# Kernel tuning notes

Hardware: AMD Instinct MI355X
Metric: run time of the kernel (lower is better)

## Reference

```python
import jax, jax.numpy as jnp
import numpy as np
import math

EMB = 1024
H = 8          # num_heads
HD = EMB // H // 2  # head_dim = 64
LAMBDA_INIT = 0.8
B, N = 2, 2048


def setup_inputs() -> dict:
    key = jax.random.key(0)
    ks = jax.random.split(key, 16)
    s = 1.0 / math.sqrt(EMB)
    d = {
        'q': jax.random.normal(ks[0], (B, N, EMB), jnp.float32),
        'k': jax.random.normal(ks[1], (B, N, EMB), jnp.float32),
        'v': jax.random.normal(ks[2], (B, N, EMB), jnp.float32),
        'Wq': jax.random.uniform(ks[3], (EMB, EMB), jnp.float32, -s, s),
        'bq': jax.random.uniform(ks[4], (EMB,), jnp.float32, -s, s),
        'Wk': jax.random.uniform(ks[5], (EMB, EMB), jnp.float32, -s, s),
        'bk': jax.random.uniform(ks[6], (EMB,), jnp.float32, -s, s),
        'Wv': jax.random.uniform(ks[7], (EMB, EMB), jnp.float32, -s, s),
        'bv': jax.random.uniform(ks[8], (EMB,), jnp.float32, -s, s),
        'Wo': jax.random.uniform(ks[9], (EMB, EMB), jnp.float32, -s, s),
        'bo': jax.random.uniform(ks[10], (EMB,), jnp.float32, -s, s),
        'lambda_q1': 0.1 * jax.random.normal(ks[11], (HD,), jnp.float32),
        'lambda_k1': 0.1 * jax.random.normal(ks[12], (HD,), jnp.float32),
        'lambda_q2': 0.1 * jax.random.normal(ks[13], (HD,), jnp.float32),
        'lambda_k2': 0.1 * jax.random.normal(ks[14], (HD,), jnp.float32),
    }
    return d


def reference(q, k, v, Wq, bq, Wk, bk, Wv, bv, Wo, bo,
              lambda_q1, lambda_k1, lambda_q2, lambda_k2):
    b, n, _ = q.shape
    # projections (torch Linear: x @ W.T + b)
    qp = q @ Wq.T + bq            # [b, n, EMB]
    kp = k @ Wk.T + bk
    vp = v @ Wv.T + bv
    # split into 2*H sub-heads of width HD for q/k; H heads of width 2*HD for v
    qh = qp.reshape(b, n, 2 * H, HD).transpose(0, 2, 1, 3)   # [b, 2H, n, HD]
    kh = kp.reshape(b, n, 2 * H, HD).transpose(0, 2, 1, 3)   # [b, 2H, n, HD]
    vh = vp.reshape(b, n, H, 2 * HD).transpose(0, 2, 1, 3)   # [b, H, n, 2HD]
    scale = 1.0 / math.sqrt(HD)
    attn = jnp.einsum('bhqd,bhkd->bhqk', qh, kh) * scale      # [b, 2H, n, n]
    attn = jax.nn.softmax(attn, axis=-1)
    lam1 = jnp.exp(jnp.sum(lambda_q1 * lambda_k1))
    lam2 = jnp.exp(jnp.sum(lambda_q2 * lambda_k2))
    lam = lam1 - lam2 + LAMBDA_INIT
    attn = attn.reshape(b, H, 2, n, n)
    diff = attn[:, :, 0] - lam * attn[:, :, 1]                # [b, H, n, n]
    out = jnp.einsum('bhqk,bhkd->bhqd', diff, vh)             # [b, H, n, 2HD]
    out = out.transpose(0, 2, 1, 3).reshape(b, n, H * 2 * HD)
    return out @ Wo.T + bo
```

## Files before the change

kernel.cpp:

```cpp
#include <hip/hip_runtime.h>
#include <stdint.h>


typedef __attribute__((ext_vector_type(8))) __bf16 bf16x8;
typedef __attribute__((ext_vector_type(4))) __bf16 bf16x4;
typedef __attribute__((ext_vector_type(4))) float f32x4;
typedef __attribute__((ext_vector_type(8))) unsigned short u16x8;
typedef __attribute__((ext_vector_type(4))) unsigned short u16x4;
typedef unsigned short u16;
typedef unsigned int u32;

#define EMB 1024
#define NSEQ 2048
#define NBATCH 2
#define NHEAD 8
#define MROWS (NBATCH*NSEQ)
#define QSCALE 0.18033688011112042f

__device__ __forceinline__ u16x4 pk4(float a, float b, float c, float d){
  bf16x4 h; h[0]=(__bf16)a; h[1]=(__bf16)b; h[2]=(__bf16)c; h[3]=(__bf16)d;
  return __builtin_bit_cast(u16x4, h);
}
__device__ __forceinline__ u16 bf1(float f){
  __bf16 h = (__bf16)f; return __builtin_bit_cast(unsigned short, h);
}

__device__ __forceinline__ bf16x8 ld8(const u16* p){
  return __builtin_bit_cast(bf16x8, *(const u16x8*)p);
}

__device__ __forceinline__ void glds16(const u16* g, u16* l){
  __builtin_amdgcn_global_load_lds(
      (const __attribute__((address_space(1))) u32*)g,
      (__attribute__((address_space(3))) u32*)l, 16, 0, 0);
}

__global__ void cvt_k(const float* __restrict__ q, const float* __restrict__ k,
                      const float* __restrict__ v, const float* __restrict__ Wq,
                      const float* __restrict__ Wk, const float* __restrict__ Wv,
                      const float* __restrict__ Wo,
                      u16* qb, u16* kb, u16* vb, u16* Wqb, u16* Wkb, u16* Wvb, u16* Wob)
{
  const int NQ4 = (NBATCH*NSEQ*EMB)/4;
  const int NW4 = (EMB*EMB)/4;
  const int total = 3*NQ4 + 4*NW4;
  for (int i = blockIdx.x*blockDim.x + threadIdx.x; i < total; i += gridDim.x*blockDim.x){
    const float* src; u16* dst; int off;
    if (i < 3*NQ4){
      int t = i / NQ4; off = i - t*NQ4;
      src = t==0 ? q : (t==1 ? k : v);
      dst = t==0 ? qb : (t==1 ? kb : vb);
    } else {
      int j = i - 3*NQ4;
      int t = j / NW4; off = j - t*NW4;
      src = t==0 ? Wq : (t==1 ? Wk : (t==2 ? Wv : Wo));
      dst = t==0 ? Wqb : (t==1 ? Wkb : (t==2 ? Wvb : Wob));
    }
    f32x4 f = *((const f32x4*)src + off);
    *((u16x4*)dst + off) = pk4(f[0], f[1], f[2], f[3]);
  }
}

__global__ void lambda_k(const float* __restrict__ lq1, const float* __restrict__ lk1,
                         const float* __restrict__ lq2, const float* __restrict__ lk2,
                         float* lam)
{
  int l = threadIdx.x;
  float p1 = lq1[l]*lk1[l];
  float p2 = lq2[l]*lk2[l];
  #pragma unroll
  for (int m=1; m<64; m<<=1){ p1 += __shfl_xor(p1, m, 64); p2 += __shfl_xor(p2, m, 64); }
  if (l==0) lam[0] = __expf(p1) - __expf(p2) + 0.8f;
}

__device__ __forceinline__ void gemm_core(
    const u16* __restrict__ A, const u16* __restrict__ W, const float* __restrict__ bias,
    u16* __restrict__ Ybf, u16* __restrict__ Yvt, float* __restrict__ Yf, int mode,
    float oscale, u16* As, u16* Bs)
{
  const int tid = threadIdx.x, w = tid >> 6, l = tid & 63;
  const int l15 = l & 15, lg = l >> 4;
  const int m0 = blockIdx.y * 128, n0 = blockIdx.x * 128;
  const int wr = w >> 1, wc = w & 1;
  const int srow = w*16 + (l >> 2);
  const int skel = (l & 3) * 8;

  f32x4 acc[4][4] = {};

  for (int kt = 0; kt < EMB/32; ++kt){
    const int kb = kt*32 + skel;
    glds16(A + (size_t)(m0 + srow)*EMB + kb,      As + w*512);
    glds16(A + (size_t)(m0 + 64 + srow)*EMB + kb, As + 2048 + w*512);
    glds16(W + (size_t)(n0 + srow)*EMB + kb,      Bs + w*512);
    glds16(W + (size_t)(n0 + 64 + srow)*EMB + kb, Bs + 2048 + w*512);
    __syncthreads();

    bf16x8 af[4], bfr[4];
    #pragma unroll
    for (int mi=0; mi<4; ++mi) af[mi]  = ld8(As + (wr*64 + mi*16 + l15)*32 + lg*8);
    #pragma unroll
    for (int ni=0; ni<4; ++ni) bfr[ni] = ld8(Bs + (wc*64 + ni*16 + l15)*32 + lg*8);
    #pragma unroll
    for (int mi=0; mi<4; ++mi)
      #pragma unroll
      for (int ni=0; ni<4; ++ni)
        acc[mi][ni] = __builtin_amdgcn_mfma_f32_16x16x32_bf16(af[mi], bfr[ni], acc[mi][ni], 0,0,0);
    __syncthreads();
  }

  #pragma unroll
  for (int mi=0; mi<4; ++mi){
    const int mr = m0 + wr*64 + mi*16 + lg*4;
    #pragma unroll
    for (int ni=0; ni<4; ++ni){
      const int nc = n0 + wc*64 + ni*16 + l15;
      const float bvs = bias[nc]*oscale;
      if (mode == 0){
        #pragma unroll
        for (int i=0;i<4;++i) Ybf[(size_t)(mr+i)*EMB + nc] = bf1(fmaf(acc[mi][ni][i], oscale, bvs));
      } else if (mode == 1){
        const int h = nc >> 7, vd = nc & 127, bb = mr >> 11, t = mr & 2047;
        u16x4 pkv = pk4(acc[mi][ni][0]+bvs, acc[mi][ni][1]+bvs,
                        acc[mi][ni][2]+bvs, acc[mi][ni][3]+bvs);
        *(u16x4*)(Yvt + ((size_t)((bb*NHEAD + h)*128 + vd))*NSEQ + t) = pkv;
      } else {
        #pragma unroll
        for (int i=0;i<4;++i) Yf[(size_t)(mr+i)*EMB + nc] = acc[mi][ni][i] + bvs;
      }
    }
  }
}

__global__ __launch_bounds__(256) void gemm_qkv(
    const u16* qb, const u16* kb, const u16* vb,
    const u16* Wqb, const u16* Wkb, const u16* Wvb,
    const float* bq, const float* bk, const float* bv,
    u16* Qp, u16* Kp, u16* Vt)
{
  __shared__ __align__(16) u16 As[4096], Bs[4096];
  const int z = blockIdx.z;
  const u16* A = z==0 ? qb : (z==1 ? kb : vb);
  const u16* W = z==0 ? Wqb : (z==1 ? Wkb : Wvb);
  const float* bias = z==0 ? bq : (z==1 ? bk : bv);
  if (z == 0)      gemm_core(A, W, bias, Qp, nullptr, nullptr, 0, QSCALE, As, Bs);
  else if (z == 1) gemm_core(A, W, bias, Kp, nullptr, nullptr, 0, 1.0f, As, Bs);
  else             gemm_core(A, W, bias, nullptr, Vt, nullptr, 1, 1.0f, As, Bs);
}

__global__ __launch_bounds__(256) void gemm_out_k(
    const u16* Xc, const u16* Wob, const float* bo, float* out)
{
  __shared__ __align__(16) u16 As[4096], Bs[4096];
  gemm_core(Xc, Wob, bo, nullptr, nullptr, out, 2, 1.0f, As, Bs);
}

__global__ __launch_bounds__(512, 4) void attn_k(
    const u16* __restrict__ Qp, const u16* __restrict__ Kp,
    const u16* __restrict__ Vt, const float* __restrict__ lamp,
    u16* __restrict__ Xc)
{
  __shared__ __align__(16) u16 shm[40960];
  u16* ldsK = shm;
  u16* ldsV = shm + 16384;
  u16* ldsP = shm + 32768;

  const int tid = threadIdx.x, w = tid >> 6, l = tid & 63;
  const int l15 = l & 15, lg = l >> 4;
  const int g = w >> 2, qg = w & 3;
  int bid = blockIdx.x;
  bid = (bid & 7)*64 + (bid >> 3);
  const int qt = bid & 31, bh = bid >> 5;
  const int b = bh >> 3, h = bh & 7;
  const int q0 = qt*64 + qg*16;

  const u16* Kg = Kp + ((size_t)b*NSEQ)*EMB + h*128;
  const u16* Vg = Vt + ((size_t)((b*NHEAD + h)*128))*NSEQ;

  const u16* qbase = Qp + (size_t)(b*NSEQ + q0 + l15)*EMB + 2*h*64;
  bf16x8 qa[2][2];
  #pragma unroll
  for (int s2=0; s2<2; ++s2)
    #pragma unroll
    for (int ks=0; ks<2; ++ks)
      qa[s2][ks] = ld8(qbase + s2*64 + ks*32 + lg*8);

  f32x4 acc[2][8] = {};
  float m_run[2] = {-1e30f, -1e30f}, l_run[2] = {0.f, 0.f};

  u16* Pw = ldsP + w*1024;
  const int sigP = (l15 >> 1) & 3;

  const int kr = l >> 4, kc = l & 15;
  const int vr = l >> 3, vh = (l >> 2) & 1, vs = l & 3;

  auto STAGE = [&](int cur, int t){
    const u16* kg = Kg + ((size_t)t*32)*EMB;
    u16* kd = ldsK + (g*2 + cur)*4096;
    #pragma unroll
    for (int j=0;j<2;++j){
      int row = qg*8 + j*4 + kr;
      glds16(kg + (size_t)row*EMB + ((kc ^ (row&7))*8), kd + (qg*8 + j*4)*128);
    }
    const u16* vg = Vg + t*32;
    u16* vd2 = ldsV + (g*2 + cur)*4096;
    #pragma unroll
    for (int j=0;j<2;++j){
      int row = qg*16 + j*8 + vr;
      glds16(vg + (size_t)(2*row + vh)*NSEQ + ((vs ^ (row&3))*8), vd2 + (qg*16 + j*8)*64);
    }
  };

  STAGE(0, g);
  __syncthreads();
  int cur = 0;

  for (int i = 0; i < 32; ++i){
    const int t = 2*i + g;
    if (i+1 < 32) STAGE(cur^1, t+2);

    const u16* Kb = ldsK + (g*2 + cur)*4096;
    const u16* Vb = ldsV + (g*2 + cur)*4096;

    #pragma unroll
    for (int s2=0; s2<2; ++s2){
      f32x4 st[2] = {};
      __builtin_amdgcn_s_setprio(1);
      #pragma unroll
      for (int nt=0; nt<2; ++nt)
        #pragma unroll
        for (int ks=0; ks<2; ++ks){
          bf16x8 kf = ld8(Kb + (nt*16 + l15)*128 + (((s2*8 + ks*4 + lg) ^ (l15&7))*8));
          st[nt] = __builtin_amdgcn_mfma_f32_16x16x32_bf16(kf, qa[s2][ks], st[nt], 0,0,0);
        }
      __builtin_amdgcn_s_setprio(0);

      float tm = fmaxf(fmaxf(st[0][0], st[0][1]), fmaxf(st[0][2], st[0][3]));
      tm = fmaxf(tm, fmaxf(fmaxf(st[1][0], st[1][1]), fmaxf(st[1][2], st[1][3])));
      tm = fmaxf(tm, __shfl_xor(tm, 16, 64));
      tm = fmaxf(tm, __shfl_xor(tm, 32, 64));
      if (!__all(tm <= m_run[s2] + 11.5f)){
        float mn = fmaxf(m_run[s2], tm);
        float al = exp2f(m_run[s2] - mn);
        m_run[s2] = mn;
        l_run[s2] *= al;
        #pragma unroll
        for (int vt=0; vt<8; ++vt){
          acc[s2][vt][0]*=al; acc[s2][vt][1]*=al; acc[s2][vt][2]*=al; acc[s2][vt][3]*=al;
        }
      }
      float ssum = 0.f;
      #pragma unroll
      for (int nt=0; nt<2; ++nt)
        #pragma unroll
        for (int ii=0; ii<4; ++ii){
          float pv = exp2f(st[nt][ii] - m_run[s2]);
          st[nt][ii] = pv; ssum += pv;
        }
      ssum += __shfl_xor(ssum, 16, 64);
      ssum += __shfl_xor(ssum, 32, 64);
      l_run[s2] += ssum;

      #pragma unroll
      for (int nt=0; nt<2; ++nt){
        u16x4 pkv = pk4(st[nt][0], st[nt][1], st[nt][2], st[nt][3]);
        *(u16x4*)(Pw + s2*512 + l15*32 + (((2*nt + (lg>>1)) ^ sigP)*8) + (lg&1)*4) = pkv;
      }
    }

    bf16x8 pa0 = ld8(Pw +       l15*32 + ((lg ^ sigP)*8));
    bf16x8 pa1 = ld8(Pw + 512 + l15*32 + ((lg ^ sigP)*8));

    __builtin_amdgcn_s_setprio(1);
    #pragma unroll
    for (int vt=0; vt<8; ++vt){
      int r = vt*8 + (l15 >> 1);
      bf16x8 vf = ld8(Vb + r*64 + (l15&1)*32 + ((lg ^ (r&3))*8));
      acc[0][vt] = __builtin_amdgcn_mfma_f32_16x16x32_bf16(vf, pa0, acc[0][vt], 0,0,0);
      acc[1][vt] = __builtin_amdgcn_mfma_f32_16x16x32_bf16(vf, pa1, acc[1][vt], 0,0,0);
    }
    __builtin_amdgcn_s_setprio(0);

    __syncthreads();
    cur ^= 1;
  }

  float* pool = (float*)shm;
  float* ml   = pool + 16896;

  if (g == 1){
    #pragma unroll
    for (int s2=0; s2<2; ++s2){
      #pragma unroll
      for (int vt=0; vt<8; ++vt)
        *(f32x4*)(pool + (size_t)(((qg*2+s2)*16 + l15))*132 + vt*16 + lg*4) = acc[s2][vt];
      if (lg == 0){
        ml[(((qg*2+s2)*16 + l15))*2 + 0] = m_run[s2];
        ml[(((qg*2+s2)*16 + l15))*2 + 1] = l_run[s2];
      }
    }
  }
  __syncthreads();
  if (g == 0){
    const float lam = lamp[0];
    float sc0[2], sc1[2];
    #pragma unroll
    for (int s2=0; s2<2; ++s2){
      float m1 = ml[(((qg*2+s2)*16 + l15))*2 + 0];
      float l1 = ml[(((qg*2+s2)*16 + l15))*2 + 1];
      float M  = fmaxf(m_run[s2], m1);
      float a0 = exp2f(m_run[s2] - M), a1 = exp2f(m1 - M);
      float L  = l_run[s2]*a0 + l1*a1;
      float f  = (s2 == 0) ? 1.f : lam;
      sc0[s2] = f*a0/L; sc1[s2] = f*a1/L;
    }
    #pragma unroll
    for (int vt=0; vt<8; ++vt){
      f32x4 c0 = *(f32x4*)(pool + (size_t)((qg*2+0)*16 + l15)*132 + vt*16 + lg*4);
      f32x4 c1 = *(f32x4*)(pool + (size_t)((qg*2+1)*16 + l15)*132 + vt*16 + lg*4);
      u16x4 o = pk4(
        acc[0][vt][0]*sc0[0] + c0[0]*sc1[0] - acc[1][vt][0]*sc0[1] - c1[0]*sc1[1],
        acc[0][vt][1]*sc0[0] + c0[1]*sc1[0] - acc[1][vt][1]*sc0[1] - c1[1]*sc1[1],
        acc[0][vt][2]*sc0[0] + c0[2]*sc1[0] - acc[1][vt][2]*sc0[1] - c1[2]*sc1[1],
        acc[0][vt][3]*sc0[0] + c0[3]*sc1[0] - acc[1][vt][3]*sc0[1] - c1[3]*sc1[1]);
      *(u16x4*)(Xc + (size_t)(b*NSEQ + q0 + l15)*EMB + h*128 + vt*16 + lg*4) = o;
    }
  }
}

extern "C" void kernel_launch(void* const* d_in, const int* in_sizes, int n_in,
                              void* d_out, int out_size, void* d_ws, size_t ws_size,
                              hipStream_t stream)
{
  const float* q   = (const float*)d_in[0];
  const float* k   = (const float*)d_in[1];
  const float* v   = (const float*)d_in[2];
  const float* Wq  = (const float*)d_in[3];
  const float* bq  = (const float*)d_in[4];
  const float* Wk  = (const float*)d_in[5];
  const float* bk  = (const float*)d_in[6];
  const float* Wv  = (const float*)d_in[7];
  const float* bv  = (const float*)d_in[8];
  const float* Wo  = (const float*)d_in[9];
  const float* bo  = (const float*)d_in[10];
  const float* lq1 = (const float*)d_in[11];
  const float* lk1 = (const float*)d_in[12];
  const float* lq2 = (const float*)d_in[13];
  const float* lk2 = (const float*)d_in[14];

  const size_t NQ = (size_t)MROWS*EMB;
  const size_t NW = (size_t)EMB*EMB;
  u16* qb  = (u16*)d_ws;
  u16* kb  = qb + NQ;
  u16* vb  = kb + NQ;
  u16* Wqb = vb + NQ;
  u16* Wkb = Wqb + NW;
  u16* Wvb = Wkb + NW;
  u16* Wob = Wvb + NW;
  u16* Qp  = Wob + NW;
  u16* Kp  = Qp + NQ;
  u16* Vt  = Kp + NQ;
  u16* Xc  = Vt + NQ;
  float* lam = (float*)(Xc + NQ);

  cvt_k<<<2048, 256, 0, stream>>>(q, k, v, Wq, Wk, Wv, Wo,
                                  qb, kb, vb, Wqb, Wkb, Wvb, Wob);
  lambda_k<<<1, 64, 0, stream>>>(lq1, lk1, lq2, lk2, lam);
  gemm_qkv<<<dim3(EMB/128, MROWS/128, 3), 256, 0, stream>>>(
      qb, kb, vb, Wqb, Wkb, Wvb, bq, bk, bv, Qp, Kp, Vt);
  attn_k<<<dim3(NBATCH*NHEAD*(NSEQ/64)), 512, 0, stream>>>(Qp, Kp, Vt, lam, Xc);
  gemm_out_k<<<dim3(EMB/128, MROWS/128), 256, 0, stream>>>(Xc, Wob, bo, (float*)d_out);
}
```

Measured before the change: 172.7 us.

## Switch attention kernel to 32x32x16 MFMA with register-resident P via permlane swap

Rewrites the attention inner loop to use 32x32x16 bf16 MFMA tiles, with each wave owning one sub-head (s) and 32 query rows instead of both sub-heads over 16 rows. The softmax probabilities are converted with v_cvt_pk_bf16_f32 and rearranged across lanes with v_permlane32_swap, so the P tile stays in registers and the LDS round trip for P is gone. K/V staging swizzles change to match, LDS grows to 66.5 KB, and the epilogue gains extra passes through LDS and extra barriers to combine the two sub-heads with lambda. The larger LDS footprint and higher register use from 4x16 accumulators may reduce occupancy under the (512,4) launch bound.

```diff
diff --git a/kernel.cpp b/kernel.cpp
--- a/kernel.cpp
+++ b/kernel.cpp
@@ -5,8 +5,10 @@
 typedef __attribute__((ext_vector_type(8))) __bf16 bf16x8;
 typedef __attribute__((ext_vector_type(4))) __bf16 bf16x4;
 typedef __attribute__((ext_vector_type(4))) float f32x4;
+typedef __attribute__((ext_vector_type(16))) float f32x16;
 typedef __attribute__((ext_vector_type(8))) unsigned short u16x8;
 typedef __attribute__((ext_vector_type(4))) unsigned short u16x4;
+typedef __attribute__((ext_vector_type(4))) unsigned int u32x4;
 typedef unsigned short u16;
 typedef unsigned int u32;
 
@@ -23,6 +25,9 @@
 }
 __device__ __forceinline__ u16 bf1(float f){
   __bf16 h = (__bf16)f; return __builtin_bit_cast(unsigned short, h);
+}
+__device__ __forceinline__ u32 cvtpk(float lo, float hi){
+  u32 r; asm("v_cvt_pk_bf16_f32 %0, %1, %2" : "=v"(r) : "v"(lo), "v"(hi)); return r;
 }
 
 __device__ __forceinline__ bf16x8 ld8(const u16* p){
@@ -159,54 +164,47 @@
     const u16* __restrict__ Vt, const float* __restrict__ lamp,
     u16* __restrict__ Xc)
 {
-  __shared__ __align__(16) u16 shm[40960];
-  u16* ldsK = shm;
-  u16* ldsV = shm + 16384;
-  u16* ldsP = shm + 32768;
+  __shared__ __align__(16) char shm[66560];
+  u16* ldsK = (u16*)shm;
+  u16* ldsV = (u16*)(shm + 32768);
 
   const int tid = threadIdx.x, w = tid >> 6, l = tid & 63;
-  const int l15 = l & 15, lg = l >> 4;
-  const int g = w >> 2, qg = w & 3;
+  const int l31 = l & 31, hl = l >> 5;
+  const int qg = w & 1, s = (w >> 1) & 1, g = w >> 2;
+  const int wg = w & 3;
   int bid = blockIdx.x;
   bid = (bid & 7)*64 + (bid >> 3);
   const int qt = bid & 31, bh = bid >> 5;
   const int b = bh >> 3, h = bh & 7;
-  const int q0 = qt*64 + qg*16;
+  const int q0 = qt*64 + qg*32;
 
   const u16* Kg = Kp + ((size_t)b*NSEQ)*EMB + h*128;
   const u16* Vg = Vt + ((size_t)((b*NHEAD + h)*128))*NSEQ;
 
-  const u16* qbase = Qp + (size_t)(b*NSEQ + q0 + l15)*EMB + 2*h*64;
-  bf16x8 qa[2][2];
+  {
+  }
+  const u16* qbase = Qp + (size_t)(b*NSEQ + q0 + l31)*EMB + (2*h + s)*64;
+  bf16x8 qa[4];
   #pragma unroll
-  for (int s2=0; s2<2; ++s2)
-    #pragma unroll
-    for (int ks=0; ks<2; ++ks)
-      qa[s2][ks] = ld8(qbase + s2*64 + ks*32 + lg*8);
-
-  f32x4 acc[2][8] = {};
-  float m_run[2] = {-1e30f, -1e30f}, l_run[2] = {0.f, 0.f};
-
-  u16* Pw = ldsP + w*1024;
-  const int sigP = (l15 >> 1) & 3;
-
-  const int kr = l >> 4, kc = l & 15;
-  const int vr = l >> 3, vh = (l >> 2) & 1, vs = l & 3;
+  for (int ks=0; ks<4; ++ks) qa[ks] = ld8(qbase + ks*16 + hl*8);
+
+  f32x16 acc[4] = {};
+  float m_run = -1e30f, l_run = 0.f;
 
   auto STAGE = [&](int cur, int t){
-    const u16* kg = Kg + ((size_t)t*32)*EMB;
+    const u16* kg = Kg + (size_t)t*32*EMB;
     u16* kd = ldsK + (g*2 + cur)*4096;
     #pragma unroll
     for (int j=0;j<2;++j){
-      int row = qg*8 + j*4 + kr;
-      glds16(kg + (size_t)row*EMB + ((kc ^ (row&7))*8), kd + (qg*8 + j*4)*128);
+      int row = wg*8 + j*4 + (l >> 4);
+      glds16(kg + (size_t)row*EMB + (((l&15) ^ (row&15))*8), kd + (wg*8 + j*4)*128);
     }
     const u16* vg = Vg + t*32;
     u16* vd2 = ldsV + (g*2 + cur)*4096;
     #pragma unroll
     for (int j=0;j<2;++j){
-      int row = qg*16 + j*8 + vr;
-      glds16(vg + (size_t)(2*row + vh)*NSEQ + ((vs ^ (row&3))*8), vd2 + (qg*16 + j*8)*64);
+      int row = wg*32 + j*16 + (l >> 2);
+      glds16(vg + (size_t)row*NSEQ + (((l&3) ^ ((row>>1)&3))*8), vd2 + (wg*32 + j*16)*32);
     }
   };
 
@@ -215,69 +213,64 @@
   int cur = 0;
 
   for (int i = 0; i < 32; ++i){
-    const int t = 2*i + g;
-    if (i+1 < 32) STAGE(cur^1, t+2);
+    if (i+1 < 32) STAGE(cur^1, 2*(i+1) + g);
 
     const u16* Kb = ldsK + (g*2 + cur)*4096;
     const u16* Vb = ldsV + (g*2 + cur)*4096;
 
-    #pragma unroll
-    for (int s2=0; s2<2; ++s2){
-      f32x4 st[2] = {};
-      __builtin_amdgcn_s_setprio(1);
-      #pragma unroll
-      for (int nt=0; nt<2; ++nt)
+    f32x16 st = {};
+    __builtin_amdgcn_s_setprio(1);
+    #pragma unroll
+    for (int ks=0; ks<4; ++ks){
+      int c = s*8 + ks*2 + hl;
+      bf16x8 kf = ld8(Kb + l31*128 + ((c ^ (l31&15))*8));
+      st = __builtin_amdgcn_mfma_f32_32x32x16_bf16(kf, qa[ks], st, 0,0,0);
+    }
+    __builtin_amdgcn_s_setprio(0);
+
+    float tm = fmaxf(st[0], st[1]);
+    #pragma unroll
+    for (int r=2; r<16; ++r) tm = fmaxf(tm, st[r]);
+    tm = fmaxf(tm, __shfl_xor(tm, 32, 64));
+    if (!__all(tm <= m_run + 11.5f)){
+      float mn = fmaxf(m_run, tm);
+      float al = exp2f(m_run - mn);
+      m_run = mn; l_run *= al;
+      #pragma unroll
+      for (int v=0; v<4; ++v)
         #pragma unroll
-        for (int ks=0; ks<2; ++ks){
-          bf16x8 kf = ld8(Kb + (nt*16 + l15)*128 + (((s2*8 + ks*4 + lg) ^ (l15&7))*8));
-          st[nt] = __builtin_amdgcn_mfma_f32_16x16x32_bf16(kf, qa[s2][ks], st[nt], 0,0,0);
-        }
-      __builtin_amdgcn_s_setprio(0);
-
-      float tm = fmaxf(fmaxf(st[0][0], st[0][1]), fmaxf(st[0][2], st[0][3]));
-      tm = fmaxf(tm, fmaxf(fmaxf(st[1][0], st[1][1]), fmaxf(st[1][2], st[1][3])));
-      tm = fmaxf(tm, __shfl_xor(tm, 16, 64));
-      tm = fmaxf(tm, __shfl_xor(tm, 32, 64));
-      if (!__all(tm <= m_run[s2] + 11.5f)){
-        float mn = fmaxf(m_run[s2], tm);
-        float al = exp2f(m_run[s2] - mn);
-        m_run[s2] = mn;
-        l_run[s2] *= al;
-        #pragma unroll
-        for (int vt=0; vt<8; ++vt){
-          acc[s2][vt][0]*=al; acc[s2][vt][1]*=al; acc[s2][vt][2]*=al; acc[s2][vt][3]*=al;
-        }
-      }
-      float ssum = 0.f;
-      #pragma unroll
-      for (int nt=0; nt<2; ++nt)
-        #pragma unroll
-        for (int ii=0; ii<4; ++ii){
-          float pv = exp2f(st[nt][ii] - m_run[s2]);
-          st[nt][ii] = pv; ssum += pv;
-        }
-      ssum += __shfl_xor(ssum, 16, 64);
-      ssum += __shfl_xor(ssum, 32, 64);
-      l_run[s2] += ssum;
-
-      #pragma unroll
-      for (int nt=0; nt<2; ++nt){
-        u16x4 pkv = pk4(st[nt][0], st[nt][1], st[nt][2], st[nt][3]);
-        *(u16x4*)(Pw + s2*512 + l15*32 + (((2*nt + (lg>>1)) ^ sigP)*8) + (lg&1)*4) = pkv;
-      }
-    }
-
-    bf16x8 pa0 = ld8(Pw +       l15*32 + ((lg ^ sigP)*8));
-    bf16x8 pa1 = ld8(Pw + 512 + l15*32 + ((lg ^ sigP)*8));
+        for (int r=0; r<16; ++r) acc[v][r] *= al;
+    }
+    float p[16];
+    float ssum = 0.f;
+    #pragma unroll
+    for (int r=0; r<16; ++r){ p[r] = exp2f(st[r] - m_run); ssum += p[r]; }
+    ssum += __shfl_xor(ssum, 32, 64);
+    l_run += ssum;
+
+    bf16x8 pa[2];
+    #pragma unroll
+    for (int kb=0; kb<2; ++kb){
+      u32 w0 = cvtpk(p[8*kb+0], p[8*kb+1]);
+      u32 w1 = cvtpk(p[8*kb+2], p[8*kb+3]);
+      u32 w2 = cvtpk(p[8*kb+4], p[8*kb+5]);
+      u32 w3 = cvtpk(p[8*kb+6], p[8*kb+7]);
+      asm volatile("v_permlane32_swap_b32 %0, %1" : "+v"(w0), "+v"(w2));
+      asm volatile("v_permlane32_swap_b32 %0, %1" : "+v"(w1), "+v"(w3));
+      u32x4 t4; t4[0]=w0; t4[1]=w1; t4[2]=w2; t4[3]=w3;
+      pa[kb] = __builtin_bit_cast(bf16x8, t4);
+    }
 
     __builtin_amdgcn_s_setprio(1);
     #pragma unroll
-    for (int vt=0; vt<8; ++vt){
-      int r = vt*8 + (l15 >> 1);
-      bf16x8 vf = ld8(Vb + r*64 + (l15&1)*32 + ((lg ^ (r&3))*8));
-      acc[0][vt] = __builtin_amdgcn_mfma_f32_16x16x32_bf16(vf, pa0, acc[0][vt], 0,0,0);
-      acc[1][vt] = __builtin_amdgcn_mfma_f32_16x16x32_bf16(vf, pa1, acc[1][vt], 0,0,0);
-    }
+    for (int kb=0; kb<2; ++kb)
+      #pragma unroll
+      for (int v=0; v<4; ++v){
+        int row = v*32 + l31;
+        int kc = kb*2 + hl;
+        bf16x8 vf = ld8(Vb + row*32 + ((kc ^ ((row>>1)&3))*8));
+        acc[v] = __builtin_amdgcn_mfma_f32_32x32x16_bf16(vf, pa[kb], acc[v], 0,0,0);
+      }
     __builtin_amdgcn_s_setprio(0);
 
     __syncthreads();
@@ -285,45 +278,65 @@
   }
 
   float* pool = (float*)shm;
-  float* ml   = pool + 16896;
+  float* ml   = (float*)(shm + 65536);
+  const int slot = qg*2 + s;
 
   if (g == 1){
     #pragma unroll
-    for (int s2=0; s2<2; ++s2){
-      #pragma unroll
-      for (int vt=0; vt<8; ++vt)
-        *(f32x4*)(pool + (size_t)(((qg*2+s2)*16 + l15))*132 + vt*16 + lg*4) = acc[s2][vt];
-      if (lg == 0){
-        ml[(((qg*2+s2)*16 + l15))*2 + 0] = m_run[s2];
-        ml[(((qg*2+s2)*16 + l15))*2 + 1] = l_run[s2];
-      }
+    for (int v=0; v<4; ++v)
+      #pragma unroll
+      for (int rr=0; rr<4; ++rr){
+        f32x4 t4; t4[0]=acc[v][rr*4+0]; t4[1]=acc[v][rr*4+1];
+        t4[2]=acc[v][rr*4+2]; t4[3]=acc[v][rr*4+3];
+        *(f32x4*)(pool + (((slot*4 + v)*4 + rr)*64 + l)*4) = t4;
+      }
+    if (hl == 0){
+      ml[(slot*32 + l31)*2 + 0] = m_run;
+      ml[(slot*32 + l31)*2 + 1] = l_run;
     }
   }
   __syncthreads();
+  float L = 1.f;
   if (g == 0){
-    const float lam = lamp[0];
-    float sc0[2], sc1[2];
-    #pragma unroll
-    for (int s2=0; s2<2; ++s2){
-      float m1 = ml[(((qg*2+s2)*16 + l15))*2 + 0];
-      float l1 = ml[(((qg*2+s2)*16 + l15))*2 + 1];
-      float M  = fmaxf(m_run[s2], m1);
-      float a0 = exp2f(m_run[s2] - M), a1 = exp2f(m1 - M);
-      float L  = l_run[s2]*a0 + l1*a1;
-      float f  = (s2 == 0) ? 1.f : lam;
-      sc0[s2] = f*a0/L; sc1[s2] = f*a1/L;
-    }
-    #pragma unroll
-    for (int vt=0; vt<8; ++vt){
-      f32x4 c0 = *(f32x4*)(pool + (size_t)((qg*2+0)*16 + l15)*132 + vt*16 + lg*4);
-      f32x4 c1 = *(f32x4*)(pool + (size_t)((qg*2+1)*16 + l15)*132 + vt*16 + lg*4);
-      u16x4 o = pk4(
-        acc[0][vt][0]*sc0[0] + c0[0]*sc1[0] - acc[1][vt][0]*sc0[1] - c1[0]*sc1[1],
-        acc[0][vt][1]*sc0[0] + c0[1]*sc1[0] - acc[1][vt][1]*sc0[1] - c1[1]*sc1[1],
-        acc[0][vt][2]*sc0[0] + c0[2]*sc1[0] - acc[1][vt][2]*sc0[1] - c1[2]*sc1[1],
-        acc[0][vt][3]*sc0[0] + c0[3]*sc1[0] - acc[1][vt][3]*sc0[1] - c1[3]*sc1[1]);
-      *(u16x4*)(Xc + (size_t)(b*NSEQ + q0 + l15)*EMB + h*128 + vt*16 + lg*4) = o;
-    }
+    float pm = ml[(slot*32 + l31)*2 + 0];
+    float pl = ml[(slot*32 + l31)*2 + 1];
+    float M  = fmaxf(m_run, pm);
+    float a0 = exp2f(m_run - M), a1 = exp2f(pm - M);
+    L = l_run*a0 + pl*a1;
+    #pragma unroll
+    for (int v=0; v<4; ++v)
+      #pragma unroll
+      for (int rr=0; rr<4; ++rr){
+        f32x4 c = *(f32x4*)(pool + (((slot*4 + v)*4 + rr)*64 + l)*4);
+        #pragma unroll
+        for (int e=0; e<4; ++e) acc[v][rr*4+e] = acc[v][rr*4+e]*a0 + c[e]*a1;
+      }
+  }
+  __syncthreads();
+  if (g == 0 && s == 1){
+    const float f = lamp[0] / L;
+    #pragma unroll
+    for (int v=0; v<4; ++v)
+      #pragma unroll
+      for (int rr=0; rr<4; ++rr){
+        f32x4 t4; t4[0]=acc[v][rr*4+0]*f; t4[1]=acc[v][rr*4+1]*f;
+        t4[2]=acc[v][rr*4+2]*f; t4[3]=acc[v][rr*4+3]*f;
+        *(f32x4*)(pool + (((qg*4 + v)*4 + rr)*64 + l)*4) = t4;
+      }
+  }
+  __syncthreads();
+  if (g == 0 && s == 0){
+    const float i0 = 1.f / L;
+    #pragma unroll
+    for (int v=0; v<4; ++v)
+      #pragma unroll
+      for (int rr=0; rr<4; ++rr){
+        f32x4 c = *(f32x4*)(pool + (((qg*4 + v)*4 + rr)*64 + l)*4);
+        u16x4 o = pk4(acc[v][rr*4+0]*i0 - c[0], acc[v][rr*4+1]*i0 - c[1],
+                      acc[v][rr*4+2]*i0 - c[2], acc[v][rr*4+3]*i0 - c[3]);
+        const int col = v*32 + rr*8 + hl*4;
+        *(u16x4*)(Xc + (size_t)(b*NSEQ + q0 + l31)*EMB + h*128 + col) = o;
+      }
   }
 }
 
```

After: 163.5 us. 1.06x faster.
